# Kernel optimization log

Hardware: AMD Instinct MI355X
Metric: run time of the kernel (lower is better)

The kernel has to match this reference:

```python
import jax, jax.numpy as jnp
import numpy as np

N_SLOTS = 24   # n_slots from __init__
N_ITERS = 25   # fixed Lloyd iterations (stand-in for sklearn max_iter/convergence)
NORM_EPS = 1e-12  # torch F.normalize eps


def setup_inputs() -> dict:
    key = jax.random.key(0)
    features = jax.random.normal(key, (32, 4096, 256), dtype=jnp.float32)
    return {"features": features}


def _pairwise_sqdist(x, x_sq, centers):
    # x: [B,N,D], x_sq: [B,N,1], centers: [B,K,D] -> [B,N,K]
    c_sq = jnp.sum(centers * centers, axis=-1)  # [B,K]
    return x_sq - 2.0 * jnp.einsum('bnd,bkd->bnk', x, centers) + c_sq[:, None, :]


def _kmeans_batched(x, k, n_iters):
    # x: [B,N,D] -> centers [B,K,D], assignments [B,N]
    B, N, D = x.shape
    # deterministic init: K evenly-spaced points per batch item
    init_idx = jnp.linspace(0, N - 1, k).astype(jnp.int32)
    centers0 = x[:, init_idx, :]  # [B,K,D]
    x_sq = jnp.sum(x * x, axis=-1, keepdims=True)  # [B,N,1]

    def step(centers, _):
        d = _pairwise_sqdist(x, x_sq, centers)          # [B,N,K]
        assign = jnp.argmin(d, axis=-1)                 # [B,N]
        onehot = jax.nn.one_hot(assign, k, dtype=x.dtype)  # [B,N,K]
        counts = jnp.sum(onehot, axis=1)                # [B,K]
        sums = jnp.einsum('bnk,bnd->bkd', onehot, x)    # [B,K,D] scatter-mean numerator
        new_centers = sums / jnp.maximum(counts, 1.0)[..., None]
        # empty clusters keep their previous center
        new_centers = jnp.where(counts[..., None] > 0, new_centers, centers)
        return new_centers, None

    centers, _ = jax.lax.scan(step, centers0, None, length=n_iters)
    final_assign = jnp.argmin(_pairwise_sqdist(x, x_sq, centers), axis=-1)
    return centers, final_assign


def reference(features):
    # L2-normalize along feature dim (use_l2_normalization=True)
    norm = jnp.sqrt(jnp.sum(features * features, axis=-1, keepdims=True))
    f = features / jnp.maximum(norm, NORM_EPS)
    # original detaches before clustering (sklearn on CPU): no gradient flow
    f = jax.lax.stop_gradient(f)
    centers, assign = _kmeans_batched(f, N_SLOTS, N_ITERS)
    # slot masks: one_hot then transpose(-2,-1) -> [B, K, N] float32
    slot_masks = jax.nn.one_hot(assign, N_SLOTS, dtype=jnp.float32).transpose(0, 2, 1)
    return centers, slot_masks
```

## Files before the change

### kernel.cpp

```cpp
#include <hip/hip_runtime.h>
#include <math.h>


#define BATCH 32
#define NPTS 4096
#define DIM 256
#define NSLOT 24
#define NITER 25

__global__ __launch_bounds__(256) void k_norm(const float* __restrict__ feat,
                                              double* __restrict__ inv_norm) {
  int lane = threadIdx.x & 63;
  int wid = threadIdx.x >> 6;
  int p = blockIdx.x * 4 + wid;
  const float4 v = *(const float4*)(feat + (size_t)p * DIM + lane * 4);
  double s = (double)v.x * v.x + (double)v.y * v.y + (double)v.z * v.z + (double)v.w * v.w;
#pragma unroll
  for (int m = 32; m; m >>= 1) s += __shfl_xor(s, m);
  if (lane == 0) inv_norm[p] = 1.0 / fmax(sqrt(s), 1e-12);
}

__device__ __forceinline__ double block_sum_256(double v, double* red) {
#pragma unroll
  for (int m = 32; m; m >>= 1) v += __shfl_xor(v, m);
  int w = threadIdx.x >> 6;
  if ((threadIdx.x & 63) == 0) red[w] = v;
  __syncthreads();
  return red[0] + red[1] + red[2] + red[3];
}

__global__ __launch_bounds__(256) void k_init_centers(const float* __restrict__ feat,
                                                      const double* __restrict__ inv_norm,
                                                      double* __restrict__ centers,
                                                      float* __restrict__ cT32,
                                                      float* __restrict__ c_sq32) {
  __shared__ double red[4];
  int t = threadIdx.x, k = blockIdx.x, b = blockIdx.y;
  int idx = (int)((double)k * (NPTS - 1) / (NSLOT - 1));
  double v = (double)feat[((size_t)b * NPTS + idx) * DIM + t] * inv_norm[b * NPTS + idx];
  centers[((size_t)b * NSLOT + k) * DIM + t] = v;
  cT32[((size_t)b * DIM + t) * NSLOT + k] = (float)v;
  double s = block_sum_256(v * v, red);
  if (t == 0) c_sq32[b * NSLOT + k] = (float)s;
}

__global__ __launch_bounds__(256) void k_transpose(const float* __restrict__ feat,
                                                   float* __restrict__ xT) {
  __shared__ float tile[64][65];
  int ix = threadIdx.x & 63, iy = threadIdx.x >> 6;
  int bx = blockIdx.x, by = blockIdx.y, b = blockIdx.z;
  const float* fb = feat + ((size_t)b * NPTS + bx * 64) * DIM + by * 64;
#pragma unroll
  for (int r = 0; r < 64; r += 4)
    tile[r + iy][ix] = fb[(size_t)(r + iy) * DIM + ix];
  __syncthreads();
  float* xb = xT + ((size_t)b * DIM + by * 64) * NPTS + bx * 64;
#pragma unroll
  for (int r = 0; r < 64; r += 4)
    xb[(size_t)(r + iy) * NPTS + ix] = tile[ix][r + iy];
}

template <bool USE_T>
__global__ __launch_bounds__(256) void k_assign(const float* __restrict__ feat,
                                                const float* __restrict__ xT,
                                                const double* __restrict__ inv_norm,
                                                const float* __restrict__ cT32,
                                                const float* __restrict__ c_sq32,
                                                int* __restrict__ assign) {
  __shared__ float part[3][64][NSLOT + 1];
  int lane = threadIdx.x & 63;
  int q = __builtin_amdgcn_readfirstlane(threadIdx.x >> 6);
  int blk = blockIdx.x, b = blockIdx.y;
  int n = blk * 64 + lane;
  const float* cb = cT32 + ((size_t)b * DIM + q * 64) * NSLOT;

  float dot[NSLOT];
#pragma unroll
  for (int k = 0; k < NSLOT; ++k) dot[k] = 0.0f;

  for (int d = 0; d < 64; d += 4) {
    float x0, x1, x2, x3;
    if (USE_T) {
      const float* xp = xT + ((size_t)b * DIM + q * 64 + d) * NPTS + n;
      x0 = xp[0]; x1 = xp[NPTS]; x2 = xp[2 * NPTS]; x3 = xp[3 * NPTS];
    } else {
      float4 v = *(const float4*)(feat + ((size_t)b * NPTS + n) * DIM + q * 64 + d);
      x0 = v.x; x1 = v.y; x2 = v.z; x3 = v.w;
    }
    const float* cp = cb + (size_t)d * NSLOT;
#pragma unroll
    for (int k = 0; k < NSLOT; ++k) {
      float s = dot[k];
      s = fmaf(x0, cp[k], s);
      s = fmaf(x1, cp[NSLOT + k], s);
      s = fmaf(x2, cp[2 * NSLOT + k], s);
      s = fmaf(x3, cp[3 * NSLOT + k], s);
      dot[k] = s;
    }
  }

  if (q) {
#pragma unroll
    for (int k = 0; k < NSLOT; ++k) part[q - 1][lane][k] = dot[k];
  }
  __syncthreads();

  if (q == 0) {
    float inv = (float)inv_norm[b * NPTS + n];
    const float* csq = c_sq32 + b * NSLOT;
    int a = 0;
    float best = 0.0f;
#pragma unroll
    for (int k = 0; k < NSLOT; ++k) {
      float df = dot[k] + part[0][lane][k] + part[1][lane][k] + part[2][lane][k];
      float s = csq[k] - 2.0f * (df * inv);
      if (k == 0) { best = s; }
      else if (s < best) { best = s; a = k; }
    }
    assign[b * NPTS + n] = a;
  }
}

__global__ __launch_bounds__(256) void k_cluster(const float* __restrict__ feat,
                                                 const double* __restrict__ inv_norm,
                                                 const int* __restrict__ assign,
                                                 double* __restrict__ centers,
                                                 float* __restrict__ cT32,
                                                 float* __restrict__ c_sq32) {
  __shared__ double part[4][DIM];
  __shared__ double red[4];
  __shared__ int wcnt[4];
  int k = blockIdx.x, b = blockIdx.y;
  int lane = threadIdx.x & 63;
  int w = __builtin_amdgcn_readfirstlane(threadIdx.x >> 6);

  const int* ab = assign + b * NPTS + w * 1024;
  int av[16];
#pragma unroll
  for (int j = 0; j < 16; ++j) av[j] = ab[lane + j * 64];

  const float* fb = feat + (size_t)b * NPTS * DIM + lane * 4;
  const double* ib = inv_norm + b * NPTS;

  double a0 = 0.0, a1 = 0.0, a2 = 0.0, a3 = 0.0;
  int cnt = 0;
#pragma unroll
  for (int j = 0; j < 16; ++j) {
    unsigned long long m = __ballot(av[j] == k);
    cnt += __popcll(m);
    while (m) {
      int bit = __ffsll((long long)m) - 1;
      m &= m - 1;
      int p = __builtin_amdgcn_readfirstlane(w * 1024 + j * 64 + bit);
      double inv = ib[p];
      float4 v = *(const float4*)(fb + (size_t)p * DIM);
      a0 += (double)v.x * inv;
      a1 += (double)v.y * inv;
      a2 += (double)v.z * inv;
      a3 += (double)v.w * inv;
    }
  }

  part[w][lane * 4 + 0] = a0;
  part[w][lane * 4 + 1] = a1;
  part[w][lane * 4 + 2] = a2;
  part[w][lane * 4 + 3] = a3;
  if (lane == 0) wcnt[w] = cnt;
  __syncthreads();

  int t = threadIdx.x;
  double s = ((part[0][t] + part[1][t]) + part[2][t]) + part[3][t];
  int total = wcnt[0] + wcnt[1] + wcnt[2] + wcnt[3];

  size_t ci = ((size_t)b * NSLOT + k) * DIM + t;
  double nc = (total > 0) ? (s / (double)total) : centers[ci];
  centers[ci] = nc;
  cT32[((size_t)b * DIM + t) * NSLOT + k] = (float)nc;
  double sq = block_sum_256(nc * nc, red);
  if (t == 0) c_sq32[b * NSLOT + k] = (float)sq;
}

__global__ __launch_bounds__(256) void k_mask(const int* __restrict__ assign,
                                              float* __restrict__ masks) {
  int t = threadIdx.x, nc = blockIdx.x, k = blockIdx.y, b = blockIdx.z;
  int n = nc * 256 + t;
  masks[((size_t)b * NSLOT + k) * NPTS + n] = (assign[b * NPTS + n] == k) ? 1.0f : 0.0f;
}

__global__ __launch_bounds__(256) void k_copyc(const double* __restrict__ centers,
                                               float* __restrict__ out_centers) {
  int t = threadIdx.x, k = blockIdx.x, b = blockIdx.y;
  size_t i = ((size_t)b * NSLOT + k) * DIM + t;
  out_centers[i] = (float)centers[i];
}

extern "C" void kernel_launch(void* const* d_in, const int* in_sizes, int n_in,
                              void* d_out, int out_size, void* d_ws, size_t ws_size,
                              hipStream_t stream) {
  (void)in_sizes; (void)n_in; (void)out_size;
  const float* feat = (const float*)d_in[0];
  float* out_centers = (float*)d_out;
  float* out_masks = out_centers + (size_t)BATCH * NSLOT * DIM;

  char* ws = (char*)d_ws;
  double* inv_norm = (double*)ws; ws += (size_t)BATCH * NPTS * 8;
  double* centers  = (double*)ws; ws += (size_t)BATCH * NSLOT * DIM * 8;
  float* cT32      = (float*)ws;  ws += (size_t)BATCH * DIM * NSLOT * 4;
  float* c_sq32    = (float*)ws;  ws += (size_t)BATCH * NSLOT * 4;
  int* assign      = (int*)ws;    ws += (size_t)BATCH * NPTS * 4;
  float* xT        = (float*)ws;
  size_t need_xT = (size_t)(ws - (char*)d_ws) + (size_t)BATCH * DIM * NPTS * 4;
  bool useT = ws_size >= need_xT;

  k_norm<<<BATCH * NPTS / 4, 256, 0, stream>>>(feat, inv_norm);
  k_init_centers<<<dim3(NSLOT, BATCH), 256, 0, stream>>>(feat, inv_norm, centers,
                                                         cT32, c_sq32);
  if (useT)
    k_transpose<<<dim3(NPTS / 64, DIM / 64, BATCH), 256, 0, stream>>>(feat, xT);

  for (int it = 0; it <= NITER; ++it) {
    if (useT)
      k_assign<true><<<dim3(NPTS / 64, BATCH), 256, 0, stream>>>(feat, xT, inv_norm,
                                                                 cT32, c_sq32, assign);
    else
      k_assign<false><<<dim3(NPTS / 64, BATCH), 256, 0, stream>>>(feat, xT, inv_norm,
                                                                  cT32, c_sq32, assign);
    if (it == NITER) break;
    k_cluster<<<dim3(NSLOT, BATCH), 256, 0, stream>>>(feat, inv_norm, assign,
                                                      centers, cT32, c_sq32);
  }

  k_mask<<<dim3(NPTS / 256, NSLOT, BATCH), 256, 0, stream>>>(assign, out_masks);
  k_copyc<<<dim3(NSLOT, BATCH), 256, 0, stream>>>(centers, out_centers);
}
```

Before: 1.838 ms.

## Compact cluster member list in LDS and balance gather across waves with XCD mapping

k_cluster now first builds a compacted shared-memory list of the points assigned to cluster k. Each wave then processes an interleaved share of that list with two independent loads in flight, instead of each wave scanning a fixed quarter of the points. This removes load imbalance between waves and raises memory-level parallelism in the gather. The launch also becomes 1D, with the block index remapped so that all clusters of a batch land on the same XCD for L2 locality. The compaction adds 16 rounds of block-wide barriers, and the per-point double-precision accumulation order changes.

```diff
diff --git a/kernel.cpp b/kernel.cpp
--- a/kernel.cpp
+++ b/kernel.cpp
@@ -127,37 +127,57 @@
                                                  double* __restrict__ centers,
                                                  float* __restrict__ cT32,
                                                  float* __restrict__ c_sq32) {
+  __shared__ int list[NPTS];
+  __shared__ int wtot[4];
   __shared__ double part[4][DIM];
   __shared__ double red[4];
-  __shared__ int wcnt[4];
-  int k = blockIdx.x, b = blockIdx.y;
-  int lane = threadIdx.x & 63;
-  int w = __builtin_amdgcn_readfirstlane(threadIdx.x >> 6);
-
-  const int* ab = assign + b * NPTS + w * 1024;
-  int av[16];
-#pragma unroll
-  for (int j = 0; j < 16; ++j) av[j] = ab[lane + j * 64];
+
+  int id = blockIdx.x;
+  int xcd = id & 7;
+  int r = id >> 3;
+  int k = r % NSLOT;
+  int b = (r / NSLOT) * 8 + xcd;
+
+  int t = threadIdx.x;
+  int lane = t & 63;
+  int w = __builtin_amdgcn_readfirstlane(t >> 6);
+
+  const int* ab = assign + b * NPTS;
+  int base = 0;
+  for (int rr = 0; rr < NPTS / 256; ++rr) {
+    int a = ab[rr * 256 + t];
+    bool m = (a == k);
+    unsigned long long bal = __ballot(m);
+    int rank = __popcll(bal & ((1ull << lane) - 1ull));
+    if (lane == 0) wtot[w] = __popcll(bal);
+    __syncthreads();
+    int off = base;
+#pragma unroll
+    for (int w2 = 0; w2 < 3; ++w2)
+      if (w2 < w) off += wtot[w2];
+    if (m) list[off + rank] = rr * 256 + t;
+    base += wtot[0] + wtot[1] + wtot[2] + wtot[3];
+    __syncthreads();
+  }
+  int mcount = base;
 
   const float* fb = feat + (size_t)b * NPTS * DIM + lane * 4;
   const double* ib = inv_norm + b * NPTS;
-
   double a0 = 0.0, a1 = 0.0, a2 = 0.0, a3 = 0.0;
-  int cnt = 0;
-#pragma unroll
-  for (int j = 0; j < 16; ++j) {
-    unsigned long long m = __ballot(av[j] == k);
-    cnt += __popcll(m);
-    while (m) {
-      int bit = __ffsll((long long)m) - 1;
-      m &= m - 1;
-      int p = __builtin_amdgcn_readfirstlane(w * 1024 + j * 64 + bit);
-      double inv = ib[p];
-      float4 v = *(const float4*)(fb + (size_t)p * DIM);
-      a0 += (double)v.x * inv;
-      a1 += (double)v.y * inv;
-      a2 += (double)v.z * inv;
-      a3 += (double)v.w * inv;
+
+  for (int i = w; i < mcount; i += 8) {
+    int n0 = __builtin_amdgcn_readfirstlane(list[i]);
+    bool have1 = (i + 4) < mcount;
+    int n1 = __builtin_amdgcn_readfirstlane(have1 ? list[i + 4] : list[i]);
+    float4 v0 = *(const float4*)(fb + (size_t)n0 * DIM);
+    float4 v1 = *(const float4*)(fb + (size_t)n1 * DIM);
+    double i0 = ib[n0];
+    double i1 = ib[n1];
+    a0 += (double)v0.x * i0; a1 += (double)v0.y * i0;
+    a2 += (double)v0.z * i0; a3 += (double)v0.w * i0;
+    if (have1) {
+      a0 += (double)v1.x * i1; a1 += (double)v1.y * i1;
+      a2 += (double)v1.z * i1; a3 += (double)v1.w * i1;
     }
   }
 
@@ -165,15 +185,12 @@
   part[w][lane * 4 + 1] = a1;
   part[w][lane * 4 + 2] = a2;
   part[w][lane * 4 + 3] = a3;
-  if (lane == 0) wcnt[w] = cnt;
-  __syncthreads();
-
-  int t = threadIdx.x;
+  __syncthreads();
+
   double s = ((part[0][t] + part[1][t]) + part[2][t]) + part[3][t];
-  int total = wcnt[0] + wcnt[1] + wcnt[2] + wcnt[3];
 
   size_t ci = ((size_t)b * NSLOT + k) * DIM + t;
-  double nc = (total > 0) ? (s / (double)total) : centers[ci];
+  double nc = (mcount > 0) ? (s / (double)mcount) : centers[ci];
   centers[ci] = nc;
   cT32[((size_t)b * DIM + t) * NSLOT + k] = (float)nc;
   double sq = block_sum_256(nc * nc, red);
@@ -226,8 +243,8 @@
       k_assign<false><<<dim3(NPTS / 64, BATCH), 256, 0, stream>>>(feat, xT, inv_norm,
                                                                   cT32, c_sq32, assign);
     if (it == NITER) break;
-    k_cluster<<<dim3(NSLOT, BATCH), 256, 0, stream>>>(feat, inv_norm, assign,
-                                                      centers, cT32, c_sq32);
+    k_cluster<<<NSLOT * BATCH, 256, 0, stream>>>(feat, inv_norm, assign,
+                                                 centers, cT32, c_sq32);
   }
 
   k_mask<<<dim3(NPTS / 256, NSLOT, BATCH), 256, 0, stream>>>(assign, out_masks);
```

Measured after the change: 1.862 ms. About the same (+1.3%).
